# Kernel tuning notes

Hardware: AMD Instinct MI355X
Metric: run time of the kernel (lower is better)

Reference implementation:

```python
import jax, jax.numpy as jnp
import numpy as np

B, N, DIM, H, DH = 2, 2048, 1024, 16, 64

def setup_inputs() -> dict:
    key = jax.random.key(0)
    ks = jax.random.split(key, 7)
    s = 0.02
    return {
        "x": jax.random.normal(ks[0], (B, N, DIM), jnp.float32),
        "pos_emb": jax.random.normal(ks[1], (N, DH), jnp.float32),
        "Wq": jax.random.normal(ks[2], (DIM, H * DH), jnp.float32) * s,
        "Wk": jax.random.normal(ks[3], (DIM, H * DH), jnp.float32) * s,
        "Wv": jax.random.normal(ks[4], (DIM, H * DH), jnp.float32) * s,
        "Wo": jax.random.normal(ks[5], (H * DH, DIM), jnp.float32) * s,
        "bo": jnp.zeros((DIM,), jnp.float32),
    }

def _rotate_half(t):
    t1, t2 = jnp.split(t, 2, axis=-1)
    return jnp.concatenate([-t2, t1], axis=-1)

def _apply_rotary(t, angles):
    # t: [b,h,n,d], angles: [n,d]
    cos = jnp.cos(angles)[None, None]
    sin = jnp.sin(angles)[None, None]
    return t * cos + _rotate_half(t) * sin

def reference(x, pos_emb, Wq, Wk, Wv, Wo, bo):
    b, n, _ = x.shape
    scale = DH ** -0.5
    def split_heads(t):  # [b,n,h*d] -> [b,h,n,d]
        return t.reshape(b, n, H, DH).transpose(0, 2, 1, 3)
    q = split_heads(x @ Wq) * scale
    k = split_heads(x @ Wk)
    v = split_heads(x @ Wv)
    q = _apply_rotary(q, pos_emb)
    k = _apply_rotary(k, pos_emb)
    sim = jnp.einsum('bhid,bhjd->bhij', q, k)
    mask_value = -jnp.finfo(sim.dtype).max
    causal_mask = jnp.triu(jnp.ones((n, n), dtype=bool), 1)
    sim = jnp.where(causal_mask, mask_value, sim)
    attn = jax.nn.softmax(sim, axis=-1)
    out = jnp.einsum('bhij,bhjd->bhid', attn, v)
    out = out.transpose(0, 2, 1, 3).reshape(b, n, H * DH)
    return out @ Wo + bo
```

## Files before the change

kernel.cpp:

```cpp
#include <hip/hip_runtime.h>

#define B_   2
#define N_   2048
#define DIM_ 1024
#define H_   16
#define DH_  64
#define M_   (B_*N_)
#define QKVN (3*DIM_)

typedef __attribute__((ext_vector_type(8)))  short short8;
typedef __attribute__((ext_vector_type(4)))  float floatx4;
typedef __attribute__((ext_vector_type(16))) float floatx16;

__device__ inline unsigned short f2b(float f) {
  union { float f; unsigned u; } v; v.f = f;
  unsigned r = v.u + 0x7fffu + ((v.u >> 16) & 1u);
  return (unsigned short)(r >> 16);
}

__device__ inline unsigned cvtpk(float a, float b) {
  unsigned d;
  asm("v_cvt_pk_bf16_f32 %0, %1, %2" : "=v"(d) : "v"(a), "v"(b));
  return d;
}

__device__ inline floatx4 mfma16(short8 a, short8 b, floatx4 c) {
  return __builtin_amdgcn_mfma_f32_16x16x32_bf16(a, b, c, 0, 0, 0);
}
__device__ inline floatx16 mfma32(short8 a, short8 b, floatx16 c) {
  return __builtin_amdgcn_mfma_f32_32x32x16_bf16(a, b, c, 0, 0, 0);
}

__device__ inline int swz(int row, int byteoff) {
  return row * 64 + (((byteoff) ^ ((row & 7) << 4)) >> 1);
}

__device__ inline void gl_lds16(const void* g, void* l) {
  __builtin_amdgcn_global_load_lds((const __attribute__((address_space(1))) void*)g,
                                   (__attribute__((address_space(3))) void*)l, 16, 0, 0);
}

__device__ inline short8 u4_to_s8(unsigned a, unsigned b, unsigned c, unsigned d) {
  union { unsigned u[4]; short8 s; } v;
  v.u[0] = a; v.u[1] = b; v.u[2] = c; v.u[3] = d;
  return v.s;
}

__global__ void cast_x_kernel(const float* __restrict__ x, unsigned short* __restrict__ xb) {
  int i = blockIdx.x * 256 + threadIdx.x;
  float4 v = ((const float4*)x)[i];
  ushort4 o;
  o.x = f2b(v.x); o.y = f2b(v.y); o.z = f2b(v.z); o.w = f2b(v.w);
  ((ushort4*)xb)[i] = o;
}

__global__ void trig_kernel(const float* __restrict__ pos, float* __restrict__ cs) {
  int i = blockIdx.x * 256 + threadIdx.x;
  float a = pos[i];
  float2 v; v.x = cosf(a); v.y = sinf(a);
  ((float2*)cs)[i] = v;
}

__global__ void transpose_w_kernel(const float* __restrict__ W0, const float* __restrict__ W1,
                                   const float* __restrict__ W2, const float* __restrict__ W3,
                                   unsigned short* __restrict__ T0, unsigned short* __restrict__ T1,
                                   unsigned short* __restrict__ T2, unsigned short* __restrict__ T3) {
  int z = blockIdx.z;
  const float* W = (z == 0) ? W0 : (z == 1) ? W1 : (z == 2) ? W2 : W3;
  unsigned short* T = (z == 0) ? T0 : (z == 1) ? T1 : (z == 2) ? T2 : T3;
  __shared__ float tile[32][33];
  int x = threadIdx.x, y = threadIdx.y;
  int bx = blockIdx.x * 32, by = blockIdx.y * 32;
  #pragma unroll
  for (int i = 0; i < 32; i += 8)
    tile[y + i][x] = W[(size_t)(by + y + i) * 1024 + bx + x];
  __syncthreads();
  #pragma unroll
  for (int i = 0; i < 32; i += 8)
    T[(size_t)(bx + y + i) * 1024 + by + x] = f2b(tile[x][y + i]);
}

template <int MODE>
__global__ __launch_bounds__(256) void gemm_bt_kernel(
    const unsigned short* __restrict__ A, const unsigned short* __restrict__ BT,
    float* __restrict__ C, const float* __restrict__ bias,
    const float* __restrict__ cs,
    unsigned short* __restrict__ qb, unsigned short* __restrict__ kb,
    unsigned short* __restrict__ vtb,
    int M, int N, int K)
{
  __shared__ __align__(16) unsigned short SH[2][4096];
  unsigned short* As = &SH[0][0];
  unsigned short* Bs = &SH[1][0];
  int t = threadIdx.x;
  int lane = t & 63, wave = t >> 6;
  int wr = (wave >> 1) * 64, wc = (wave & 1) * 64;

  const unsigned short* Ab = A  + (size_t)(blockIdx.y * 128) * K;
  const unsigned short* Bb = BT + (size_t)(blockIdx.x * 128) * K;

  int sA = wave * 2;
  int grow = (lane >> 2), gcol = (lane & 3) * 8;
  const unsigned short* gA0 = Ab + (size_t)((sA    ) * 16 + grow) * K + gcol;
  const unsigned short* gA1 = Ab + (size_t)((sA + 1) * 16 + grow) * K + gcol;
  const unsigned short* gB0 = Bb + (size_t)((sA    ) * 16 + grow) * K + gcol;
  const unsigned short* gB1 = Bb + (size_t)((sA + 1) * 16 + grow) * K + gcol;
  unsigned short* lA0 = &As[(sA    ) * 512];
  unsigned short* lA1 = &As[(sA + 1) * 512];
  unsigned short* lB0 = &Bs[(sA    ) * 512];
  unsigned short* lB1 = &Bs[(sA + 1) * 512];

  floatx4 acc[4][4];
  #pragma unroll
  for (int i = 0; i < 4; ++i)
    #pragma unroll
    for (int j = 0; j < 4; ++j)
      acc[i][j] = (floatx4){0.f, 0.f, 0.f, 0.f};

  int nk = K >> 5;
  for (int kt = 0; kt < nk; ++kt) {
    if (kt) __syncthreads();
    int ko = kt * 32;
    gl_lds16(gA0 + ko, lA0);
    gl_lds16(gA1 + ko, lA1);
    gl_lds16(gB0 + ko, lB0);
    gl_lds16(gB1 + ko, lB1);
    __syncthreads();
    short8 af[4], bf[4];
    #pragma unroll
    for (int fi = 0; fi < 4; ++fi)
      af[fi] = *(const short8*)&As[(wr + fi * 16 + (lane & 15)) * 32 + (lane >> 4) * 8];
    #pragma unroll
    for (int fj = 0; fj < 4; ++fj)
      bf[fj] = *(const short8*)&Bs[(wc + fj * 16 + (lane & 15)) * 32 + (lane >> 4) * 8];
    __builtin_amdgcn_s_setprio(1);
    #pragma unroll
    for (int fi = 0; fi < 4; ++fi)
      #pragma unroll
      for (int fj = 0; fj < 4; ++fj)
        acc[fi][fj] = mfma16(af[fi], bf[fj], acc[fi][fj]);
    __builtin_amdgcn_s_setprio(0);
  }

  int lane15 = lane & 15;
  int row0 = blockIdx.y * 128 + wr + (lane >> 4) * 4;

  if constexpr (MODE == 0) {
    int col0 = blockIdx.x * 128 + wc + lane15;
    #pragma unroll
    for (int fi = 0; fi < 4; ++fi) {
      #pragma unroll
      for (int fj = 0; fj < 4; ++fj) {
        int col = col0 + fj * 16;
        float bv = bias ? bias[col] : 0.f;
        #pragma unroll
        for (int r = 0; r < 4; ++r) {
          int row = row0 + fi * 16 + r;
          C[(size_t)row * N + col] = acc[fi][fj][r] + bv;
        }
      }
    }
  } else {
    __syncthreads();
    unsigned short* ep = &SH[0][0];
    int colbase = blockIdx.x * 128 + wc;
    int region = colbase >> 10;
    int bb = (blockIdx.y * 128) >> 11;
    if (region < 2) {
      const float qs = (region == 0) ? 0.18033688011112042f : 1.0f;
      unsigned short* dstb = (region == 0) ? qb : kb;
      int h = (colbase >> 6) & 15;
      #pragma unroll
      for (int h2 = 0; h2 < 2; ++h2) {
        #pragma unroll
        for (int fi2 = 0; fi2 < 2; ++fi2) {
          int fi = h2 * 2 + fi2;
          #pragma unroll
          for (int fj = 0; fj < 4; ++fj) {
            int d = fj * 16 + lane15;
            float sgn = (fj < 2) ? -1.f : 1.f;
            #pragma unroll
            for (int r = 0; r < 4; ++r) {
              int n = (row0 + fi * 16 + r) & 2047;
              float2 csv = *(const float2*)&cs[((size_t)n * 64 + d) * 2];
              float a = acc[fi][fj][r], p = acc[fi][fj ^ 2][r];
              int nloc = fi2 * 16 + ((lane >> 4) & 3) * 4 + r;
              ep[wave * 2048 + nloc * 64 + d] = f2b((a * csv.x + sgn * p * csv.y) * qs);
            }
          }
        }
        __syncthreads();
        {
          int r2 = lane >> 1, half = lane & 1;
          int n_glob = blockIdx.y * 128 + wr + h2 * 32 + r2;
          int nn = n_glob & 2047;
          unsigned short* dst = dstb + (((size_t)(bb * 16 + h)) * 2048 + nn) * 64 + half * 32;
          const unsigned short* srcp = ep + wave * 2048 + r2 * 64 + half * 32;
          #pragma unroll
          for (int c = 0; c < 4; ++c)
            *(int4*)(dst + c * 8) = *(const int4*)(srcp + c * 8);
        }
        __syncthreads();
      }
    } else {
      int n0 = (blockIdx.y * 128) & 2047;
      int hA = ((blockIdx.x * 128) >> 6) & 15;
      #pragma unroll
      for (int nh = 0; nh < 2; ++nh) {
        if ((wave >> 1) == nh) {
          #pragma unroll
          for (int fi = 0; fi < 4; ++fi) {
            #pragma unroll
            for (int fj = 0; fj < 4; ++fj) {
              int d = fj * 16 + lane15;
              int sw = (d & 7) << 3;
              #pragma unroll
              for (int r = 0; r < 4; ++r) {
                int nl = fi * 16 + ((lane >> 4) & 3) * 4 + r;
                ep[(wave & 1) * 4096 + d * 64 + (nl ^ sw)] = f2b(acc[fi][fj][r]);
              }
            }
          }
        }
        __syncthreads();
        {
          int hh = t >> 7, d = (t >> 1) & 63, half = t & 1;
          int sw = (d & 7) << 3;
          const unsigned short* srcp = ep + hh * 4096 + d * 64;
          unsigned short* dst = vtb + (((size_t)(bb * 16 + hA + hh)) * 64 + d) * 2048
                                    + n0 + nh * 64 + half * 32;
          #pragma unroll
          for (int c = 0; c < 4; ++c) {
            int off = (half * 32 + c * 8) ^ sw;
            *(int4*)(dst + c * 8) = *(const int4*)(srcp + off);
          }
        }
        __syncthreads();
      }
    }
  }
}

__global__ __launch_bounds__(512, 4) void attn_kernel(
    const unsigned short* __restrict__ qg, const unsigned short* __restrict__ kg,
    const unsigned short* __restrict__ vtg, unsigned short* __restrict__ ctx)
{
  __shared__ __align__(16) unsigned short KV[4][4096];
  __shared__ float lrbuf[4][32];

  int bid = blockIdx.x;
  int bh  = bid & 31;
  int qc  = (bid < 256) ? (15 - (bid >> 5)) : ((bid - 256) >> 5);
  int t = threadIdx.x, lane = t & 63, wave = t >> 6;
  int s = wave >> 1, kvh = wave & 1;
  int lane31 = lane & 31, hi = lane >> 5;
  bool hib = (hi != 0);
  int b = bh >> 4, h = bh & 15;

  const unsigned short* kp = kg  + (size_t)bh * N_ * DH_;
  const unsigned short* vp = vtg + (size_t)bh * 64 * (size_t)N_;

  int srow = t >> 3;
  int sc16 = (t & 7) * 16;
  int4 kreg, vreg;

#define LOAD_TILE(KV0) do {                                                    \
    kreg = *(const int4*)(kp + (size_t)((KV0) + srow) * 64 + (sc16 >> 1));     \
    vreg = *(const int4*)(vp + (size_t)srow * N_ + (KV0) + (sc16 >> 1));       \
  } while (0)
#define STORE_TILE(BUF) do {                                                   \
    *(int4*)&KV[(BUF)][swz(srow, sc16)]     = kreg;                            \
    *(int4*)&KV[2 + (BUF)][swz(srow, sc16)] = vreg;                            \
  } while (0)

  int q0 = qc * 128;
  int nt = (qc + 1) * 2;
  int qw0 = q0 + s * 32;
  int qr  = qw0 + lane31;

  short8 qf[4];
  {
    const unsigned short* qrp = qg + ((size_t)bh * N_ + qr) * DH_;
    #pragma unroll
    for (int ks = 0; ks < 4; ++ks)
      qf[ks] = *(const short8*)(qrp + ks * 16 + hi * 8);
  }

  LOAD_TILE(0);
  STORE_TILE(0);

  floatx16 oa0 = (floatx16)(0.f), oa1 = (floatx16)(0.f);
  float lr = 0.f;

  for (int kt = 0; kt < nt; ++kt) {
    __syncthreads();
    int kv0 = kt * 64;
    bool more = (kt + 1 < nt);
    if (more) LOAD_TILE(kv0 + 64);

    int kvbase = kv0 + kvh * 32;
    bool active = (kvbase <= qw0 + 31);
    if (active) {
      const unsigned short* Kb = KV[kt & 1];
      const unsigned short* Vb = KV[2 + (kt & 1)];

      floatx16 sa = (floatx16)(0.f);
      __builtin_amdgcn_s_setprio(1);
      #pragma unroll
      for (int ks = 0; ks < 4; ++ks) {
        short8 kf = *(const short8*)&Kb[swz(kvh * 32 + lane31, ks * 32 + hi * 16)];
        sa = mfma32(kf, qf[ks], sa);
      }
      __builtin_amdgcn_s_setprio(0);

      if (kvbase + 31 > qw0) {
        #pragma unroll
        for (int r = 0; r < 16; ++r) {
          int kvA = kvbase + ((r & 3) + 8 * (r >> 2) + 4 * hi);
          if (kvA > qr) sa[r] = -3.0e38f;
        }
      }

      float ps = 0.f;
      #pragma unroll
      for (int r = 0; r < 16; ++r) {
        float p = exp2f(sa[r]); sa[r] = p; ps += p;
      }
      ps += __shfl_xor(ps, 32);
      lr += ps;

      unsigned pk0 = cvtpk(sa[0],  sa[1]),  pk1 = cvtpk(sa[2],  sa[3]);
      unsigned pk2 = cvtpk(sa[4],  sa[5]),  pk3 = cvtpk(sa[6],  sa[7]);
      unsigned pk4 = cvtpk(sa[8],  sa[9]),  pk5 = cvtpk(sa[10], sa[11]);
      unsigned pk6 = cvtpk(sa[12], sa[13]), pk7 = cvtpk(sa[14], sa[15]);
      unsigned t0 = hib ? pk0 : pk2, t1 = hib ? pk1 : pk3;
      unsigned t2 = hib ? pk4 : pk6, t3 = hib ? pk5 : pk7;
      unsigned r0 = (unsigned)__shfl_xor((int)t0, 32);
      unsigned r1 = (unsigned)__shfl_xor((int)t1, 32);
      unsigned r2 = (unsigned)__shfl_xor((int)t2, 32);
      unsigned r3 = (unsigned)__shfl_xor((int)t3, 32);
      unsigned o0 = hib ? pk2 : pk0, o1 = hib ? pk3 : pk1;
      unsigned o2 = hib ? pk6 : pk4, o3 = hib ? pk7 : pk5;
      short8 pa = u4_to_s8(hib ? r0 : o0, hib ? r1 : o1, hib ? o0 : r0, hib ? o1 : r1);
      short8 pb = u4_to_s8(hib ? r2 : o2, hib ? r3 : o3, hib ? o2 : r2, hib ? o3 : r3);

      int vb0 = kvh * 64;
      short8 v00 = *(const short8*)&Vb[swz(lane31,      vb0 + hi * 16)];
      short8 v01 = *(const short8*)&Vb[swz(32 + lane31, vb0 + hi * 16)];
      short8 v10 = *(const short8*)&Vb[swz(lane31,      vb0 + 32 + hi * 16)];
      short8 v11 = *(const short8*)&Vb[swz(32 + lane31, vb0 + 32 + hi * 16)];
      __builtin_amdgcn_s_setprio(1);
      oa0 = mfma32(v00, pa, oa0);
      oa1 = mfma32(v01, pa, oa1);
      oa0 = mfma32(v10, pb, oa0);
      oa1 = mfma32(v11, pb, oa1);
      __builtin_amdgcn_s_setprio(0);
    }

    if (more) STORE_TILE((kt + 1) & 1);
  }

  __syncthreads();
  float* F = (float*)&KV[0][0];
  int fsw = (lane31 & 7) << 2;
  if (kvh == 1) {
    #pragma unroll
    for (int r = 0; r < 16; ++r) {
      int d = (r & 3) + 8 * (r >> 2) + 4 * hi;
      F[s * 2048 + lane31 * 64 + (d ^ fsw)]        = oa0[r];
      F[s * 2048 + lane31 * 64 + ((32 + d) ^ fsw)] = oa1[r];
    }
    if (!hib) lrbuf[s][lane31] = lr;
  }
  __syncthreads();
  if (kvh == 0) {
    float inv = 1.0f / (lr + lrbuf[s][lane31]);
    #pragma unroll
    for (int r = 0; r < 16; ++r) {
      int d = (r & 3) + 8 * (r >> 2) + 4 * hi;
      oa0[r] = (oa0[r] + F[s * 2048 + lane31 * 64 + (d ^ fsw)])        * inv;
      oa1[r] = (oa1[r] + F[s * 2048 + lane31 * 64 + ((32 + d) ^ fsw)]) * inv;
    }
  }
  __syncthreads();
  if (kvh == 0) {
    int qrow = s * 32 + lane31;
    #pragma unroll
    for (int db = 0; db < 2; ++db) {
      floatx16 ov = (db == 0) ? oa0 : oa1;
      #pragma unroll
      for (int a = 0; a < 4; ++a) {
        unsigned w0 = cvtpk(ov[4 * a + 0], ov[4 * a + 1]);
        unsigned w1 = cvtpk(ov[4 * a + 2], ov[4 * a + 3]);
        int byteoff = 64 * db + 16 * a + 8 * hi;
        uint2 val; val.x = w0; val.y = w1;
        *(uint2*)&KV[qrow >> 6][(qrow & 63) * 64 + ((byteoff ^ ((qrow & 7) << 4)) >> 1)] = val;
      }
    }
  }
  __syncthreads();
  {
    int r = t >> 2, q4 = (t & 3) * 32;
    const unsigned short* srow_ = &KV[r >> 6][(r & 63) * 64];
    unsigned short* dst = ctx + (size_t)(b * N_ + q0 + r) * DIM_ + h * 64 + (q4 >> 1);
    #pragma unroll
    for (int c = 0; c < 2; ++c) {
      int byteo = q4 + c * 16;
      int4 v = *(const int4*)&srow_[(byteo ^ ((r & 7) << 4)) >> 1];
      *(int4*)(dst + c * 8) = v;
    }
  }
#undef LOAD_TILE
#undef STORE_TILE
}

extern "C" void kernel_launch(void* const* d_in, const int* in_sizes, int n_in,
                              void* d_out, int out_size, void* d_ws, size_t ws_size,
                              hipStream_t stream)
{
  const float* x   = (const float*)d_in[0];
  const float* pos = (const float*)d_in[1];
  const float* Wq  = (const float*)d_in[2];
  const float* Wk  = (const float*)d_in[3];
  const float* Wv  = (const float*)d_in[4];
  const float* Wo  = (const float*)d_in[5];
  const float* bo  = (const float*)d_in[6];
  float* out = (float*)d_out;

  char* w = (char*)d_ws;
  size_t off = 0;
  auto alloc = [&](size_t bytes) {
    char* p = w + off;
    off += (bytes + 255) & ~(size_t)255;
    return p;
  };
  unsigned short* xb  = (unsigned short*)alloc((size_t)M_ * DIM_ * 2);
  unsigned short* WT  = (unsigned short*)alloc((size_t)QKVN * DIM_ * 2);
  unsigned short* WoT = (unsigned short*)alloc((size_t)DIM_ * DIM_ * 2);
  float* cs = (float*)alloc((size_t)N_ * DH_ * 2 * 4);
  unsigned short* qb  = (unsigned short*)alloc((size_t)B_ * H_ * N_ * DH_ * 2);
  unsigned short* kb  = (unsigned short*)alloc((size_t)B_ * H_ * N_ * DH_ * 2);
  unsigned short* vtb = (unsigned short*)alloc((size_t)B_ * H_ * N_ * DH_ * 2);
  unsigned short* ctx = (unsigned short*)alloc((size_t)M_ * DIM_ * 2);

  cast_x_kernel<<<(M_ * DIM_ / 4) / 256, 256, 0, stream>>>(x, xb);
  trig_kernel<<<(N_ * DH_) / 256, 256, 0, stream>>>(pos, cs);
  transpose_w_kernel<<<dim3(32, 32, 4), dim3(32, 8), 0, stream>>>(
      Wq, Wk, Wv, Wo,
      WT, WT + (size_t)DIM_ * DIM_, WT + (size_t)2 * DIM_ * DIM_, WoT);
  gemm_bt_kernel<1><<<dim3(QKVN / 128, M_ / 128), 256, 0, stream>>>(
      xb, WT, nullptr, nullptr, cs, qb, kb, vtb, M_, QKVN, DIM_);
  attn_kernel<<<512, 512, 0, stream>>>(qb, kb, vtb, ctx);
  gemm_bt_kernel<0><<<dim3(DIM_ / 128, M_ / 128), 256, 0, stream>>>(
      ctx, WoT, out, bo, nullptr, nullptr, nullptr, nullptr, M_, DIM_, DIM_);
}
```

Before: 214.2 us.

## Double-buffer LDS in GEMM main loop and swizzle block order across XCDs

The GEMM kernel now keeps two LDS buffers and issues the global-to-LDS loads for the next K tile before computing on the current one. This cuts the loop to one barrier per iteration and lets load latency overlap the MFMA work. It also remaps the flat block index so that consecutive blocks land on the same XCD group, aiming for better L2 reuse. The cost is double the LDS footprint, which may lower occupancy. The remap assumes the block count is divisible by 8.

```diff
diff --git a/kernel.cpp b/kernel.cpp
--- a/kernel.cpp
+++ b/kernel.cpp
@@ -89,15 +89,18 @@
     unsigned short* __restrict__ vtb,
     int M, int N, int K)
 {
-  __shared__ __align__(16) unsigned short SH[2][4096];
-  unsigned short* As = &SH[0][0];
-  unsigned short* Bs = &SH[1][0];
+  __shared__ __align__(16) unsigned short SH[2][2][4096];
   int t = threadIdx.x;
   int lane = t & 63, wave = t >> 6;
   int wr = (wave >> 1) * 64, wc = (wave & 1) * 64;
 
-  const unsigned short* Ab = A  + (size_t)(blockIdx.y * 128) * K;
-  const unsigned short* Bb = BT + (size_t)(blockIdx.x * 128) * K;
+  int flat = blockIdx.y * gridDim.x + blockIdx.x;
+  int cpx  = (gridDim.x * gridDim.y) >> 3;
+  int swzf = (flat & 7) * cpx + (flat >> 3);
+  int bx = swzf % gridDim.x, by = swzf / gridDim.x;
+
+  const unsigned short* Ab = A  + (size_t)(by * 128) * K;
+  const unsigned short* Bb = BT + (size_t)(bx * 128) * K;
 
   int sA = wave * 2;
   int grow = (lane >> 2), gcol = (lane & 3) * 8;
@@ -105,10 +108,13 @@
   const unsigned short* gA1 = Ab + (size_t)((sA + 1) * 16 + grow) * K + gcol;
   const unsigned short* gB0 = Bb + (size_t)((sA    ) * 16 + grow) * K + gcol;
   const unsigned short* gB1 = Bb + (size_t)((sA + 1) * 16 + grow) * K + gcol;
-  unsigned short* lA0 = &As[(sA    ) * 512];
-  unsigned short* lA1 = &As[(sA + 1) * 512];
-  unsigned short* lB0 = &Bs[(sA    ) * 512];
-  unsigned short* lB1 = &Bs[(sA + 1) * 512];
+
+#define STAGE(bf, kt) do { int ko = (kt) * 32;                                 \
+    gl_lds16(gA0 + ko, &SH[bf][0][(sA    ) * 512]);                            \
+    gl_lds16(gA1 + ko, &SH[bf][0][(sA + 1) * 512]);                            \
+    gl_lds16(gB0 + ko, &SH[bf][1][(sA    ) * 512]);                            \
+    gl_lds16(gB1 + ko, &SH[bf][1][(sA + 1) * 512]);                            \
+  } while (0)
 
   floatx4 acc[4][4];
   #pragma unroll
@@ -118,14 +124,13 @@
       acc[i][j] = (floatx4){0.f, 0.f, 0.f, 0.f};
 
   int nk = K >> 5;
+  STAGE(0, 0);
+  __syncthreads();
   for (int kt = 0; kt < nk; ++kt) {
-    if (kt) __syncthreads();
-    int ko = kt * 32;
-    gl_lds16(gA0 + ko, lA0);
-    gl_lds16(gA1 + ko, lA1);
-    gl_lds16(gB0 + ko, lB0);
-    gl_lds16(gB1 + ko, lB1);
-    __syncthreads();
+    int cur = kt & 1;
+    if (kt + 1 < nk) STAGE(cur ^ 1, kt + 1);
+    const unsigned short* As = &SH[cur][0][0];
+    const unsigned short* Bs = &SH[cur][1][0];
     short8 af[4], bf[4];
     #pragma unroll
     for (int fi = 0; fi < 4; ++fi)
@@ -140,13 +145,15 @@
       for (int fj = 0; fj < 4; ++fj)
         acc[fi][fj] = mfma16(af[fi], bf[fj], acc[fi][fj]);
     __builtin_amdgcn_s_setprio(0);
-  }
+    __syncthreads();
+  }
+#undef STAGE
 
   int lane15 = lane & 15;
-  int row0 = blockIdx.y * 128 + wr + (lane >> 4) * 4;
+  int row0 = by * 128 + wr + (lane >> 4) * 4;
 
   if constexpr (MODE == 0) {
-    int col0 = blockIdx.x * 128 + wc + lane15;
+    int col0 = bx * 128 + wc + lane15;
     #pragma unroll
     for (int fi = 0; fi < 4; ++fi) {
       #pragma unroll
@@ -161,11 +168,10 @@
       }
     }
   } else {
-    __syncthreads();
-    unsigned short* ep = &SH[0][0];
-    int colbase = blockIdx.x * 128 + wc;
+    unsigned short* ep = &SH[0][0][0];
+    int colbase = bx * 128 + wc;
     int region = colbase >> 10;
-    int bb = (blockIdx.y * 128) >> 11;
+    int bb = (by * 128) >> 11;
     if (region < 2) {
       const float qs = (region == 0) ? 0.18033688011112042f : 1.0f;
       unsigned short* dstb = (region == 0) ? qb : kb;
@@ -192,7 +198,7 @@
         __syncthreads();
         {
           int r2 = lane >> 1, half = lane & 1;
-          int n_glob = blockIdx.y * 128 + wr + h2 * 32 + r2;
+          int n_glob = by * 128 + wr + h2 * 32 + r2;
           int nn = n_glob & 2047;
           unsigned short* dst = dstb + (((size_t)(bb * 16 + h)) * 2048 + nn) * 64 + half * 32;
           const unsigned short* srcp = ep + wave * 2048 + r2 * 64 + half * 32;
@@ -203,8 +209,8 @@
         __syncthreads();
       }
     } else {
-      int n0 = (blockIdx.y * 128) & 2047;
-      int hA = ((blockIdx.x * 128) >> 6) & 15;
+      int n0 = (by * 128) & 2047;
+      int hA = ((bx * 128) >> 6) & 15;
       #pragma unroll
       for (int nh = 0; nh < 2; ++nh) {
         if ((wave >> 1) == nh) {
```

Result: faster. 201.8 us (-5.8%).
